# Kernel optimization log

Hardware: AMD Instinct MI355X
Metric: run time of the kernel (lower is better)

## Reference

```python
import jax, jax.numpy as jnp
import numpy as np

B, S, D = 8, 1024, 768
H, DK, DV = 12, 64, 64


def setup_inputs() -> dict:
    key = jax.random.key(0)
    ks = jax.random.split(key, 8)
    s_in = 1.0 / np.sqrt(D)
    s_cat = 1.0 / np.sqrt(H * DV)
    return {
        "x": jax.random.normal(ks[0], (B, S, D), jnp.float32),
        "Wq": jax.random.normal(ks[1], (H, D, DK), jnp.float32) * s_in,
        "bq": jnp.zeros((H, DK), jnp.float32),
        "Wk": jax.random.normal(ks[2], (H, D, DK), jnp.float32) * s_in,
        "bk": jnp.zeros((H, DK), jnp.float32),
        "Wv": jax.random.normal(ks[3], (H, D, DV), jnp.float32) * s_in,
        "bv": jnp.zeros((H, DV), jnp.float32),
        "W0": jax.random.normal(ks[4], (H * DV, D), jnp.float32) * s_cat,
        "b0": jnp.zeros((D,), jnp.float32),
    }


def reference(x, Wq, bq, Wk, bk, Wv, bv, W0, b0):
    # Per-head projections, batched across heads (same math as the ModuleList loop).
    q = jnp.einsum("bsd,hdk->bhsk", x, Wq) + bq[None, :, None, :]  # [B,H,S,DK]
    k = jnp.einsum("bsd,hdk->bhsk", x, Wk) + bk[None, :, None, :]
    v = jnp.einsum("bsd,hdv->bhsv", x, Wv) + bv[None, :, None, :]
    scale = 1.0 / jnp.sqrt(jnp.asarray(DK, x.dtype))
    scores = jnp.einsum("bhqk,bhsk->bhqs", q, k) * scale  # [B,H,S,S]
    causal = jnp.tril(jnp.ones((S, S), bool))
    scores = jnp.where(causal[None, None], scores, jnp.asarray(-1e9, x.dtype))
    attn = jax.nn.softmax(scores, axis=-1)
    out = jnp.einsum("bhqs,bhsv->bhqv", attn, v)  # [B,H,S,DV]
    # concat heads along last dim -> [B,S,H*DV]
    out = jnp.transpose(out, (0, 2, 1, 3)).reshape(B, S, H * DV)
    # output projection (dropout is identity in eval mode / p=0)
    return out @ W0 + b0
```

## Files before the change

### kernel.cpp

```cpp
#include <hip/hip_runtime.h>


typedef __attribute__((ext_vector_type(8))) short short8;
typedef __attribute__((ext_vector_type(4))) short short4_t;
typedef __attribute__((ext_vector_type(4))) float f32x4;

#define Bsz 8
#define Ssz 1024
#define Dsz 768
#define Hsz 12
#define DKsz 64
#define KVB 128

__device__ __forceinline__ short f2bf(float f) {
    unsigned u = __float_as_uint(f);
    u = (u + 0x7fffu + ((u >> 16) & 1u)) >> 16;
    return (short)u;
}

__device__ __forceinline__ float fexp2(float x) {
    float r;
    asm("v_exp_f32 %0, %1" : "=v"(r) : "v"(x));
    return r;
}

__device__ __forceinline__ f32x4 mfma16(short8 a, short8 b, f32x4 c) {
    return __builtin_amdgcn_mfma_f32_16x16x32_bf16(a, b, c, 0, 0, 0);
}

__device__ __forceinline__ void gload16(const short* g, short* lds) {
    __builtin_amdgcn_global_load_lds(
        (const __attribute__((address_space(1))) void*)g,
        (__attribute__((address_space(3))) void*)lds, 16, 0, 0);
}

template <int N> __device__ __forceinline__ void waitv() {
    if constexpr (N == 8)      asm volatile("s_waitcnt vmcnt(8)" ::: "memory");
    else if constexpr (N == 4) asm volatile("s_waitcnt vmcnt(4)" ::: "memory");
    else if constexpr (N == 3) asm volatile("s_waitcnt vmcnt(3)" ::: "memory");
    else                       asm volatile("s_waitcnt vmcnt(0)" ::: "memory");
}

__global__ __launch_bounds__(256) void prep_kernel(
    const float* __restrict__ x, const float* __restrict__ Wq,
    const float* __restrict__ Wk, const float* __restrict__ Wv,
    const float* __restrict__ W0,
    short* __restrict__ xbf, short* __restrict__ Wt, short* __restrict__ W0t) {
    int bid = blockIdx.x, tid = threadIdx.x;
    if (bid < 3072) {
        int i = (bid * 256 + tid) * 8;
        float4 a = *reinterpret_cast<const float4*>(&x[i]);
        float4 b = *reinterpret_cast<const float4*>(&x[i + 4]);
        short8 o;
        o[0] = f2bf(a.x); o[1] = f2bf(a.y); o[2] = f2bf(a.z); o[3] = f2bf(a.w);
        o[4] = f2bf(b.x); o[5] = f2bf(b.y); o[6] = f2bf(b.z); o[7] = f2bf(b.w);
        *reinterpret_cast<short8*>(&xbf[i]) = o;
    } else if (bid < 9984) {
        int idx = (bid - 3072) * 256 + tid;
        int n = idx / Dsz, k = idx % Dsz;
        int which = n / 768;
        int hc = n - which * 768;
        int h = hc >> 6, c = hc & 63;
        const float* W = (which == 0) ? Wq : (which == 1) ? Wk : Wv;
        Wt[idx] = f2bf(W[(h * Dsz + k) * DKsz + c]);
    } else {
        int idx = (bid - 9984) * 256 + tid;
        int n = idx / Dsz, k = idx % Dsz;
        W0t[idx] = f2bf(W0[k * Dsz + n]);
    }
}

#define GEMM_MAINX(A_, Bt_, Kdim, MF_, NF_, AIT_, BIT_, WAITL_)                    \
    int tid = threadIdx.x, w = tid >> 6, l = tid & 63;                             \
    int wr = w >> 2, wc = w & 3;                                                   \
    int lr = l & 15, lg = l >> 4;                                                  \
    __shared__ short Als[2][(MF_ * 32) * 32];                                      \
    __shared__ short Bls[2][(NF_ * 64) * 32];                                      \
    f32x4 acc[MF_][NF_] = {};                                                      \
    auto STAGE = [&](int cb, int k0) {                                             \
        _Pragma("unroll")                                                          \
        for (int it = 0; it < (AIT_); ++it) {                                      \
            int i = it * 512 + tid;                                                \
            int r = i >> 2, sl = i & 3;                                            \
            gload16((A_) + r * (Kdim) + k0 + ((sl ^ ((r >> 1) & 3)) << 3),         \
                    &Als[cb][(it * 512 + w * 64) * 8]);                            \
        }                                                                          \
        _Pragma("unroll")                                                          \
        for (int it = 0; it < (BIT_); ++it) {                                      \
            int i = it * 512 + tid;                                                \
            int r = i >> 2, sl = i & 3;                                            \
            gload16((Bt_) + r * (Kdim) + k0 + ((sl ^ ((r >> 1) & 3)) << 3),        \
                    &Bls[cb][(it * 512 + w * 64) * 8]);                            \
        }                                                                          \
    };                                                                             \
    auto COMPUTE = [&](int cb) {                                                   \
        short8 bf[NF_];                                                            \
        _Pragma("unroll")                                                          \
        for (int n = 0; n < (NF_); ++n) {                                          \
            int row = wc * ((NF_) * 16) + n * 16 + lr;                             \
            bf[n] = *reinterpret_cast<const short8*>(                              \
                &Bls[cb][row * 32 + ((lg ^ ((row >> 1) & 3)) << 3)]);              \
        }                                                                          \
        __builtin_amdgcn_s_setprio(1);                                             \
        _Pragma("unroll")                                                          \
        for (int m = 0; m < (MF_); ++m) {                                          \
            int row = wr * ((MF_) * 16) + m * 16 + lr;                             \
            short8 af = *reinterpret_cast<const short8*>(                          \
                &Als[cb][row * 32 + ((lg ^ ((row >> 1) & 3)) << 3)]);              \
            _Pragma("unroll")                                                      \
            for (int n = 0; n < (NF_); ++n)                                        \
                acc[m][n] = mfma16(af, bf[n], acc[m][n]);                          \
        }                                                                          \
        __builtin_amdgcn_s_setprio(0);                                             \
    };                                                                             \
    STAGE(0, 0);                                                                   \
    STAGE(1, 32);                                                                  \
    for (int k = 0; k < (Kdim) / 32 - 2; ++k) {                                    \
        waitv<WAITL_>();                                                           \
        __builtin_amdgcn_s_barrier();                                              \
        COMPUTE(k & 1);                                                            \
        __builtin_amdgcn_s_barrier();                                              \
        STAGE(k & 1, (k + 2) * 32);                                                \
    }                                                                              \
    waitv<WAITL_>();                                                               \
    __builtin_amdgcn_s_barrier();                                                  \
    COMPUTE(((Kdim) / 32 - 2) & 1);                                                \
    waitv<0>();                                                                    \
    __builtin_amdgcn_s_barrier();                                                  \
    COMPUTE(((Kdim) / 32 - 1) & 1);

__global__ __launch_bounds__(512, 2) void gemm_qkv_kernel(
    const short* __restrict__ A, const short* __restrict__ Bt,
    const float* __restrict__ bq, const float* __restrict__ bk,
    const float* __restrict__ bv,
    short* __restrict__ Qb, short* __restrict__ Kb, short* __restrict__ Vb) {
    int tile = (blockIdx.x & 7) * 72 + (blockIdx.x >> 3);
    int tm = tile / 9, tn = tile % 9;
    const short* Ab = A + (size_t)tm * 128 * Dsz;
    const short* Bb = Bt + (size_t)tn * 256 * Dsz;
    GEMM_MAINX(Ab, Bb, Dsz, 4, 4, 1, 2, 3)
    int which = tn / 3;
    const float* bias = (which == 0) ? bq : (which == 1) ? bk : bv;
    int row0 = tm * 128 + wr * 64;
    int col0 = tn * 256 + wc * 64 - which * 768;
    if (which == 2) {
#pragma unroll
        for (int m = 0; m < 4; ++m)
#pragma unroll
            for (int n = 0; n < 4; ++n) {
                int s0 = row0 + m * 16 + lg * 4;
                int col = col0 + n * 16 + lr;
                int b = s0 >> 10, s = s0 & 1023;
                int h = col >> 6, c = col & 63;
                float bi = bias[h * 64 + c];
                short4_t pk;
#pragma unroll
                for (int j = 0; j < 4; ++j) pk[j] = f2bf(acc[m][n][j] + bi);
                *reinterpret_cast<short4_t*>(
                    &Vb[(((size_t)b * Hsz + h) * DKsz + c) * Ssz + s]) = pk;
            }
    } else {
        short* dst = (which == 0) ? Qb : Kb;
#pragma unroll
        for (int m = 0; m < 4; ++m)
#pragma unroll
            for (int n = 0; n < 4; ++n)
#pragma unroll
                for (int j = 0; j < 4; ++j) {
                    int row = row0 + m * 16 + lg * 4 + j;
                    int col = col0 + n * 16 + lr;
                    int b = row >> 10, s = row & 1023;
                    int h = col >> 6, c = col & 63;
                    float v = acc[m][n][j] + bias[h * 64 + c];
                    if (which == 0) v *= 0.180336884f;
                    dst[(((size_t)b * Hsz + h) * Ssz + s) * DKsz + c] = f2bf(v);
                }
    }
}

__global__ __launch_bounds__(256) void attn_kernel(const short* __restrict__ Q,
                                                   const short* __restrict__ K,
                                                   const short* __restrict__ Vt,
                                                   short* __restrict__ O) {
    int raw = blockIdx.x;
    int xcd = raw & 7, slot = raw >> 3;
    int bh  = (slot >> 4) * 8 + xcd;
    int qb  = 15 - (slot & 15);
    const short* Qh = Q + (size_t)bh * Ssz * DKsz;
    const short* Kh = K + (size_t)bh * Ssz * DKsz;
    const short* Vh = Vt + (size_t)bh * DKsz * Ssz;
    int tid = threadIdx.x, w = tid >> 6, l = tid & 63;
    int lr = l & 15, lg = l >> 4;
    __shared__ short Kls[2][KVB * 64];
    __shared__ short Vls[2][64 * KVB];
    __shared__ short Pls[4][16 * KVB];

    auto STAGEKV = [&](int cb, int t) {
        const short* Ksrc = Kh + t * KVB * 64;
#pragma unroll
        for (int it = 0; it < 4; ++it) {
            int i = it * 256 + tid;
            int r = i >> 3, ps = i & 7;
            gload16(Ksrc + r * 64 + ((ps ^ (r & 7)) << 3),
                    &Kls[cb][(it * 256 + w * 64) * 8]);
        }
#pragma unroll
        for (int it = 0; it < 4; ++it) {
            int i = it * 256 + tid;
            int r = i >> 4, ps = i & 15;
            gload16(Vh + r * Ssz + t * KVB + ((ps ^ (r & 15)) << 3),
                    &Vls[cb][(it * 256 + w * 64) * 8]);
        }
    };

    int qrow = qb * 64 + w * 16 + lr;
    short8 aq0 = *reinterpret_cast<const short8*>(&Qh[qrow * 64 + lg * 8]);
    short8 aq1 = *reinterpret_cast<const short8*>(&Qh[qrow * 64 + 32 + lg * 8]);

    short8 ones;
#pragma unroll
    for (int e = 0; e < 8; ++e) ones[e] = (short)0x3F80;

    f32x4 acc[4] = {};
    f32x4 accL = {};

    int nt = qb / 2 + 1;
    STAGEKV(0, 0);
    for (int t = 0; t < nt; ++t) {
        int cb = t & 1;
        if (t + 1 < nt) { STAGEKV(cb ^ 1, t + 1); waitv<8>(); }
        else            { waitv<0>(); }
        __builtin_amdgcn_s_barrier();

        f32x4 s[8] = {};
        __builtin_amdgcn_s_setprio(1);
#pragma unroll
        for (int n = 0; n < 8; ++n) {
            int kr = n * 16 + lr;
            short8 kf0 = *reinterpret_cast<const short8*>(
                &Kls[cb][kr * 64 + ((lg ^ (kr & 7)) << 3)]);
            short8 kf1 = *reinterpret_cast<const short8*>(
                &Kls[cb][kr * 64 + (((lg + 4) ^ (kr & 7)) << 3)]);
            s[n] = mfma16(aq0, kf0, s[n]);
            s[n] = mfma16(aq1, kf1, s[n]);
        }
        __builtin_amdgcn_s_setprio(0);

        if (t == nt - 1) {
#pragma unroll
            for (int n = 0; n < 8; ++n)
#pragma unroll
                for (int j = 0; j < 4; ++j) {
                    int kv = t * KVB + n * 16 + lr;
                    int q = qb * 64 + w * 16 + lg * 4 + j;
                    if (kv > q) s[n][j] = -1e30f;
                }
        }

#pragma unroll
        for (int n = 0; n < 8; ++n)
#pragma unroll
            for (int j = 0; j < 4; ++j) {
                float p = fexp2(s[n][j]);
                int row = lg * 4 + j;
                int col = n * 16 + lr;
                Pls[w][row * KVB + (col ^ (row << 3))] = f2bf(p);
            }

        __builtin_amdgcn_s_setprio(1);
#pragma unroll
        for (int kk = 0; kk < 4; ++kk) {
            int sl = (((kk * 4 + lg) ^ lr) << 3);
            short8 pa = *reinterpret_cast<const short8*>(&Pls[w][lr * KVB + sl]);
            accL = mfma16(pa, ones, accL);
#pragma unroll
            for (int n = 0; n < 4; ++n) {
                short8 vf = *reinterpret_cast<const short8*>(
                    &Vls[cb][(n * 16 + lr) * KVB + sl]);
                acc[n] = mfma16(pa, vf, acc[n]);
            }
        }
        __builtin_amdgcn_s_setprio(0);
        __builtin_amdgcn_s_barrier();
    }

    int b = bh / Hsz, h = bh % Hsz;
#pragma unroll
    for (int n = 0; n < 4; ++n)
#pragma unroll
        for (int j = 0; j < 4; ++j) {
            int q = qb * 64 + w * 16 + lg * 4 + j;
            int dv = n * 16 + lr;
            float o = acc[n][j] / accL[j];
            O[((size_t)(b * Ssz + q)) * Dsz + h * DKsz + dv] = f2bf(o);
        }
}

__global__ __launch_bounds__(512, 2) void gemm_out_kernel(const short* __restrict__ A,
                                                          const short* __restrict__ Bt,
                                                          const float* __restrict__ b0,
                                                          float* __restrict__ out) {
    int tile = (blockIdx.x & 7) * 24 + (blockIdx.x >> 3);
    int tm = tile / 6, tn = tile % 6;
    const short* Ab = A + (size_t)tm * 256 * Dsz;
    const short* Bb = Bt + (size_t)tn * 128 * Dsz;
    GEMM_MAINX(Ab, Bb, Dsz, 8, 2, 2, 1, 3)
    int row0 = tm * 256 + wr * 128;
    int col0 = tn * 128 + wc * 32;
#pragma unroll
    for (int m = 0; m < 8; ++m)
#pragma unroll
        for (int n = 0; n < 2; ++n)
#pragma unroll
            for (int j = 0; j < 4; ++j) {
                int row = row0 + m * 16 + lg * 4 + j;
                int col = col0 + n * 16 + lr;
                out[(size_t)row * Dsz + col] = acc[m][n][j] + b0[col];
            }
}

extern "C" void kernel_launch(void* const* d_in, const int* in_sizes, int n_in,
                              void* d_out, int out_size, void* d_ws, size_t ws_size,
                              hipStream_t stream) {
    const float* x  = (const float*)d_in[0];
    const float* Wq = (const float*)d_in[1];
    const float* bq = (const float*)d_in[2];
    const float* Wk = (const float*)d_in[3];
    const float* bk = (const float*)d_in[4];
    const float* Wv = (const float*)d_in[5];
    const float* bv = (const float*)d_in[6];
    const float* W0 = (const float*)d_in[7];
    const float* b0 = (const float*)d_in[8];
    float* out = (float*)d_out;

    const size_t N_X   = (size_t)Bsz * Ssz * Dsz;
    const size_t N_QKV = (size_t)3 * Dsz * Dsz;
    const size_t N_W0  = (size_t)Dsz * Dsz;
    const size_t N_HD  = (size_t)Bsz * Hsz * Ssz * DKsz;

    short* xbf   = (short*)d_ws;
    short* wqkvt = xbf + N_X;
    short* w0t   = wqkvt + N_QKV;
    short* Qb    = w0t + N_W0;
    short* Kb    = Qb + N_HD;
    short* Vb    = Kb + N_HD;
    short* attno = Vb + N_HD;

    prep_kernel<<<12288, 256, 0, stream>>>(x, Wq, Wk, Wv, W0, xbf, wqkvt, w0t);
    gemm_qkv_kernel<<<576, 512, 0, stream>>>(xbf, wqkvt, bq, bk, bv, Qb, Kb, Vb);
    attn_kernel<<<Bsz * Hsz * 16, 256, 0, stream>>>(Qb, Kb, Vb, attno);
    gemm_out_kernel<<<192, 512, 0, stream>>>(attno, w0t, b0, out);
}
```

Baseline: 218.6 us.

## Use LDS-tiled weight transposes and 128x128x64 GEMM tiles with deeper K step

The weight-prep stage now transposes 64x64 tiles through shared memory with vectorized float4 loads and short8 stores, replacing scalar strided gathers. Both GEMMs switch to a common 128x128 output tile with a K step of 64, an 8-way XOR swizzle, and twice as many blocks. The aim is to cut uncoalesced prep traffic, halve barrier and loop overhead per K, and fill more CUs. In exchange each block reuses each staged tile less, and the larger LDS buffers may reduce occupancy.

```diff
diff --git a/kernel.cpp b/kernel.cpp
--- a/kernel.cpp
+++ b/kernel.cpp
@@ -37,7 +37,6 @@
 template <int N> __device__ __forceinline__ void waitv() {
     if constexpr (N == 8)      asm volatile("s_waitcnt vmcnt(8)" ::: "memory");
     else if constexpr (N == 4) asm volatile("s_waitcnt vmcnt(4)" ::: "memory");
-    else if constexpr (N == 3) asm volatile("s_waitcnt vmcnt(3)" ::: "memory");
     else                       asm volatile("s_waitcnt vmcnt(0)" ::: "memory");
 }
 
@@ -46,6 +45,7 @@
     const float* __restrict__ Wk, const float* __restrict__ Wv,
     const float* __restrict__ W0,
     short* __restrict__ xbf, short* __restrict__ Wt, short* __restrict__ W0t) {
+    __shared__ float tl[64][65];
     int bid = blockIdx.x, tid = threadIdx.x;
     if (bid < 3072) {
         int i = (bid * 256 + tid) * 8;
@@ -55,99 +55,142 @@
         o[0] = f2bf(a.x); o[1] = f2bf(a.y); o[2] = f2bf(a.z); o[3] = f2bf(a.w);
         o[4] = f2bf(b.x); o[5] = f2bf(b.y); o[6] = f2bf(b.z); o[7] = f2bf(b.w);
         *reinterpret_cast<short8*>(&xbf[i]) = o;
-    } else if (bid < 9984) {
-        int idx = (bid - 3072) * 256 + tid;
-        int n = idx / Dsz, k = idx % Dsz;
-        int which = n / 768;
-        int hc = n - which * 768;
-        int h = hc >> 6, c = hc & 63;
+    } else if (bid < 3504) {
+        int b2 = bid - 3072;
+        int wh = b2 / 12, dt = b2 % 12;
+        int which = wh / 12, h = wh % 12;
         const float* W = (which == 0) ? Wq : (which == 1) ? Wk : Wv;
-        Wt[idx] = f2bf(W[(h * Dsz + k) * DKsz + c]);
+        int dr = tid >> 2, c0 = (tid & 3) * 16;
+        const float* src = &W[((size_t)(h * Dsz) + dt * 64 + dr) * DKsz + c0];
+#pragma unroll
+        for (int i = 0; i < 4; ++i) {
+            float4 v = *reinterpret_cast<const float4*>(&src[i * 4]);
+            tl[dr][c0 + i * 4 + 0] = v.x; tl[dr][c0 + i * 4 + 1] = v.y;
+            tl[dr][c0 + i * 4 + 2] = v.z; tl[dr][c0 + i * 4 + 3] = v.w;
+        }
+        __syncthreads();
+        int c = tid >> 2, dd0 = (tid & 3) * 16;
+        short8 o0, o1;
+#pragma unroll
+        for (int j = 0; j < 8; ++j) {
+            o0[j] = f2bf(tl[dd0 + j][c]);
+            o1[j] = f2bf(tl[dd0 + 8 + j][c]);
+        }
+        size_t n = (size_t)which * 768 + h * 64 + c;
+        *reinterpret_cast<short8*>(&Wt[n * Dsz + dt * 64 + dd0]) = o0;
+        *reinterpret_cast<short8*>(&Wt[n * Dsz + dt * 64 + dd0 + 8]) = o1;
     } else {
-        int idx = (bid - 9984) * 256 + tid;
-        int n = idx / Dsz, k = idx % Dsz;
-        W0t[idx] = f2bf(W0[k * Dsz + n]);
+        int b3 = bid - 3504;
+        int kt = b3 / 12, nt = b3 % 12;
+        int kr = tid >> 2, c0 = (tid & 3) * 16;
+        const float* src = &W0[((size_t)(kt * 64) + kr) * Dsz + nt * 64 + c0];
+#pragma unroll
+        for (int i = 0; i < 4; ++i) {
+            float4 v = *reinterpret_cast<const float4*>(&src[i * 4]);
+            tl[kr][c0 + i * 4 + 0] = v.x; tl[kr][c0 + i * 4 + 1] = v.y;
+            tl[kr][c0 + i * 4 + 2] = v.z; tl[kr][c0 + i * 4 + 3] = v.w;
+        }
+        __syncthreads();
+        int c = tid >> 2, kk0 = (tid & 3) * 16;
+        short8 o0, o1;
+#pragma unroll
+        for (int j = 0; j < 8; ++j) {
+            o0[j] = f2bf(tl[kk0 + j][c]);
+            o1[j] = f2bf(tl[kk0 + 8 + j][c]);
+        }
+        size_t n = (size_t)nt * 64 + c;
+        *reinterpret_cast<short8*>(&W0t[n * Dsz + kt * 64 + kk0]) = o0;
+        *reinterpret_cast<short8*>(&W0t[n * Dsz + kt * 64 + kk0 + 8]) = o1;
     }
 }
 
-#define GEMM_MAINX(A_, Bt_, Kdim, MF_, NF_, AIT_, BIT_, WAITL_)                    \
+#define GEMM_MAIN64(A_, Bt_, Kdim)                                                 \
     int tid = threadIdx.x, w = tid >> 6, l = tid & 63;                             \
     int wr = w >> 2, wc = w & 3;                                                   \
     int lr = l & 15, lg = l >> 4;                                                  \
-    __shared__ short Als[2][(MF_ * 32) * 32];                                      \
-    __shared__ short Bls[2][(NF_ * 64) * 32];                                      \
-    f32x4 acc[MF_][NF_] = {};                                                      \
+    __shared__ short Als[2][128 * 64];                                             \
+    __shared__ short Bls[2][128 * 64];                                             \
+    f32x4 acc[4][2] = {};                                                          \
     auto STAGE = [&](int cb, int k0) {                                             \
         _Pragma("unroll")                                                          \
-        for (int it = 0; it < (AIT_); ++it) {                                      \
+        for (int it = 0; it < 2; ++it) {                                           \
             int i = it * 512 + tid;                                                \
-            int r = i >> 2, sl = i & 3;                                            \
-            gload16((A_) + r * (Kdim) + k0 + ((sl ^ ((r >> 1) & 3)) << 3),         \
+            int r = i >> 3, sl = i & 7;                                            \
+            gload16((A_) + r * (Kdim) + k0 + ((sl ^ (r & 7)) << 3),                \
                     &Als[cb][(it * 512 + w * 64) * 8]);                            \
         }                                                                          \
         _Pragma("unroll")                                                          \
-        for (int it = 0; it < (BIT_); ++it) {                                      \
+        for (int it = 0; it < 2; ++it) {                                           \
             int i = it * 512 + tid;                                                \
-            int r = i >> 2, sl = i & 3;                                            \
-            gload16((Bt_) + r * (Kdim) + k0 + ((sl ^ ((r >> 1) & 3)) << 3),        \
+            int r = i >> 3, sl = i & 7;                                            \
+            gload16((Bt_) + r * (Kdim) + k0 + ((sl ^ (r & 7)) << 3),               \
                     &Bls[cb][(it * 512 + w * 64) * 8]);                            \
         }                                                                          \
     };                                                                             \
     auto COMPUTE = [&](int cb) {                                                   \
-        short8 bf[NF_];                                                            \
-        _Pragma("unroll")                                                          \
-        for (int n = 0; n < (NF_); ++n) {                                          \
-            int row = wc * ((NF_) * 16) + n * 16 + lr;                             \
-            bf[n] = *reinterpret_cast<const short8*>(                              \
-                &Bls[cb][row * 32 + ((lg ^ ((row >> 1) & 3)) << 3)]);              \
+        short8 af[4][2], bf[2][2];                                                 \
+        _Pragma("unroll")                                                          \
+        for (int n = 0; n < 2; ++n) {                                              \
+            int row = wc * 32 + n * 16 + lr;                                       \
+            _Pragma("unroll")                                                      \
+            for (int kk = 0; kk < 2; ++kk)                                         \
+                bf[n][kk] = *reinterpret_cast<const short8*>(                      \
+                    &Bls[cb][row * 64 + (((kk * 4 + lg) ^ (row & 7)) << 3)]);      \
+        }                                                                          \
+        _Pragma("unroll")                                                          \
+        for (int m = 0; m < 4; ++m) {                                              \
+            int row = wr * 64 + m * 16 + lr;                                       \
+            _Pragma("unroll")                                                      \
+            for (int kk = 0; kk < 2; ++kk)                                         \
+                af[m][kk] = *reinterpret_cast<const short8*>(                      \
+                    &Als[cb][row * 64 + (((kk * 4 + lg) ^ (row & 7)) << 3)]);      \
         }                                                                          \
         __builtin_amdgcn_s_setprio(1);                                             \
         _Pragma("unroll")                                                          \
-        for (int m = 0; m < (MF_); ++m) {                                          \
-            int row = wr * ((MF_) * 16) + m * 16 + lr;                             \
-            short8 af = *reinterpret_cast<const short8*>(                          \
-                &Als[cb][row * 32 + ((lg ^ ((row >> 1) & 3)) << 3)]);              \
+        for (int kk = 0; kk < 2; ++kk)                                             \
             _Pragma("unroll")                                                      \
-            for (int n = 0; n < (NF_); ++n)                                        \
-                acc[m][n] = mfma16(af, bf[n], acc[m][n]);                          \
-        }                                                                          \
+            for (int m = 0; m < 4; ++m)                                            \
+                _Pragma("unroll")                                                  \
+                for (int n = 0; n < 2; ++n)                                        \
+                    acc[m][n] = mfma16(af[m][kk], bf[n][kk], acc[m][n]);           \
         __builtin_amdgcn_s_setprio(0);                                             \
     };                                                                             \
+    const int ns = (Kdim) / 64;                                                    \
     STAGE(0, 0);                                                                   \
-    STAGE(1, 32);                                                                  \
-    for (int k = 0; k < (Kdim) / 32 - 2; ++k) {                                    \
-        waitv<WAITL_>();                                                           \
+    STAGE(1, 64);                                                                  \
+    for (int k = 0; k < ns - 2; ++k) {                                             \
+        waitv<4>();                                                                \
         __builtin_amdgcn_s_barrier();                                              \
         COMPUTE(k & 1);                                                            \
         __builtin_amdgcn_s_barrier();                                              \
-        STAGE(k & 1, (k + 2) * 32);                                                \
+        STAGE(k & 1, (k + 2) * 64);                                                \
     }                                                                              \
-    waitv<WAITL_>();                                                               \
+    waitv<4>();                                                                    \
     __builtin_amdgcn_s_barrier();                                                  \
-    COMPUTE(((Kdim) / 32 - 2) & 1);                                                \
+    COMPUTE(ns & 1);                                                               \
     waitv<0>();                                                                    \
     __builtin_amdgcn_s_barrier();                                                  \
-    COMPUTE(((Kdim) / 32 - 1) & 1);
+    COMPUTE((ns - 1) & 1);
 
 __global__ __launch_bounds__(512, 2) void gemm_qkv_kernel(
     const short* __restrict__ A, const short* __restrict__ Bt,
     const float* __restrict__ bq, const float* __restrict__ bk,
     const float* __restrict__ bv,
     short* __restrict__ Qb, short* __restrict__ Kb, short* __restrict__ Vb) {
-    int tile = (blockIdx.x & 7) * 72 + (blockIdx.x >> 3);
-    int tm = tile / 9, tn = tile % 9;
+    int tile = (blockIdx.x & 7) * 144 + (blockIdx.x >> 3);
+    int tm = tile / 18, tn = tile % 18;
     const short* Ab = A + (size_t)tm * 128 * Dsz;
-    const short* Bb = Bt + (size_t)tn * 256 * Dsz;
-    GEMM_MAINX(Ab, Bb, Dsz, 4, 4, 1, 2, 3)
-    int which = tn / 3;
+    const short* Bb = Bt + (size_t)tn * 128 * Dsz;
+    GEMM_MAIN64(Ab, Bb, Dsz)
+    int which = tn / 6;
     const float* bias = (which == 0) ? bq : (which == 1) ? bk : bv;
     int row0 = tm * 128 + wr * 64;
-    int col0 = tn * 256 + wc * 64 - which * 768;
+    int col0 = tn * 128 + wc * 32 - which * 768;
     if (which == 2) {
 #pragma unroll
         for (int m = 0; m < 4; ++m)
 #pragma unroll
-            for (int n = 0; n < 4; ++n) {
+            for (int n = 0; n < 2; ++n) {
                 int s0 = row0 + m * 16 + lg * 4;
                 int col = col0 + n * 16 + lr;
                 int b = s0 >> 10, s = s0 & 1023;
@@ -164,7 +207,7 @@
 #pragma unroll
         for (int m = 0; m < 4; ++m)
 #pragma unroll
-            for (int n = 0; n < 4; ++n)
+            for (int n = 0; n < 2; ++n)
 #pragma unroll
                 for (int j = 0; j < 4; ++j) {
                     int row = row0 + m * 16 + lg * 4 + j;
@@ -300,15 +343,15 @@
                                                           const short* __restrict__ Bt,
                                                           const float* __restrict__ b0,
                                                           float* __restrict__ out) {
-    int tile = (blockIdx.x & 7) * 24 + (blockIdx.x >> 3);
+    int tile = (blockIdx.x & 7) * 48 + (blockIdx.x >> 3);
     int tm = tile / 6, tn = tile % 6;
-    const short* Ab = A + (size_t)tm * 256 * Dsz;
+    const short* Ab = A + (size_t)tm * 128 * Dsz;
     const short* Bb = Bt + (size_t)tn * 128 * Dsz;
-    GEMM_MAINX(Ab, Bb, Dsz, 8, 2, 2, 1, 3)
-    int row0 = tm * 256 + wr * 128;
+    GEMM_MAIN64(Ab, Bb, Dsz)
+    int row0 = tm * 128 + wr * 64;
     int col0 = tn * 128 + wc * 32;
 #pragma unroll
-    for (int m = 0; m < 8; ++m)
+    for (int m = 0; m < 4; ++m)
 #pragma unroll
         for (int n = 0; n < 2; ++n)
 #pragma unroll
@@ -346,8 +389,8 @@
     short* Vb    = Kb + N_HD;
     short* attno = Vb + N_HD;
 
-    prep_kernel<<<12288, 256, 0, stream>>>(x, Wq, Wk, Wv, W0, xbf, wqkvt, w0t);
-    gemm_qkv_kernel<<<576, 512, 0, stream>>>(xbf, wqkvt, bq, bk, bv, Qb, Kb, Vb);
+    prep_kernel<<<3648, 256, 0, stream>>>(x, Wq, Wk, Wv, W0, xbf, wqkvt, w0t);
+    gemm_qkv_kernel<<<1152, 512, 0, stream>>>(xbf, wqkvt, bq, bk, bv, Qb, Kb, Vb);
     attn_kernel<<<Bsz * Hsz * 16, 256, 0, stream>>>(Qb, Kb, Vb, attno);
-    gemm_out_kernel<<<192, 512, 0, stream>>>(attno, w0t, b0, out);
-}
+    gemm_out_kernel<<<384, 512, 0, stream>>>(attno, w0t, b0, out);
+}
```

New measurement: 192.3 us. -12.0%, faster.
